# Optimization experiments

Hardware: AMD Instinct MI355X
Metric: run time of the kernel (lower is better)

Reference implementation:

```python
import jax, jax.numpy as jnp
import numpy as np

B, T, IN, H, OUT = 16384, 60, 1, 50, 1


def setup_inputs() -> dict:
    key = jax.random.key(0)
    ks = jax.random.split(key, 7)
    s = 1.0 / np.sqrt(H)
    return {
        "input_seq": jax.random.normal(ks[0], (B, T, IN), dtype=jnp.float32),
        "w_ih": jax.random.uniform(ks[1], (4 * H, IN), jnp.float32, -s, s),
        "w_hh": jax.random.uniform(ks[2], (4 * H, H), jnp.float32, -s, s),
        "b_ih": jax.random.uniform(ks[3], (4 * H,), jnp.float32, -s, s),
        "b_hh": jax.random.uniform(ks[4], (4 * H,), jnp.float32, -s, s),
        "w_lin": jax.random.uniform(ks[5], (OUT, H * T), jnp.float32, -s, s),
        "b_lin": jax.random.uniform(ks[6], (OUT,), jnp.float32, -s, s),
    }


def reference(input_seq, w_ih, w_hh, b_ih, b_hh, w_lin, b_lin):
    # Precompute input projections for all timesteps: [T, B, 4H]
    x_proj = jnp.einsum('bti,gi->tbg', input_seq, w_ih) + b_ih + b_hh

    def step(carry, xp):
        h, c = carry
        gates = xp + h @ w_hh.T  # [B, 4H]
        i, f, g, o = jnp.split(gates, 4, axis=-1)  # PyTorch gate order
        i, f, o = jax.nn.sigmoid(i), jax.nn.sigmoid(f), jax.nn.sigmoid(o)
        g = jnp.tanh(g)
        c = f * c + i * g
        h = o * jnp.tanh(c)
        return (h, c), h

    h0 = jnp.zeros((input_seq.shape[0], H), dtype=input_seq.dtype)
    (_, _), hs = jax.lax.scan(step, (h0, h0), x_proj)  # hs: [T, B, H]
    lstm_out = jnp.transpose(hs, (1, 0, 2)).reshape(-1, H * T)  # [B, T*H]
    return lstm_out @ w_lin.T + b_lin
```

## Files before the change

### kernel.cpp

```cpp
#include <hip/hip_runtime.h>


namespace {
constexpr int TS = 60;

typedef _Float16 half8 __attribute__((ext_vector_type(8)));
typedef _Float16 half2v __attribute__((ext_vector_type(2)));
typedef float f32x4 __attribute__((ext_vector_type(4)));

__device__ __forceinline__ float fexp2(float x) { return __builtin_amdgcn_exp2f(x); }
__device__ __forceinline__ float frcp(float x) { return __builtin_amdgcn_rcpf(x); }
__device__ __forceinline__ f32x4 mfma16(half8 a, half8 b, f32x4 c) {
  return __builtin_amdgcn_mfma_f32_16x16x32_f16(a, b, c, 0, 0, 0);
}
}

__global__ __launch_bounds__(256, 2) void lstm_t13(
    const float* __restrict__ x,
    const float* __restrict__ w_ih,
    const float* __restrict__ w_hh,
    const float* __restrict__ b_ih,
    const float* __restrict__ b_hh,
    const float* __restrict__ w_lin,
    const float* __restrict__ b_lin,
    float* __restrict__ out)
{
  __shared__ __align__(16) _Float16 Hs[2][2][16 * 64];
  __shared__ float WL[TS * 64];
  __shared__ float XL[TS * 32];
  __shared__ float OB[4][2][16];

  const int tid = threadIdx.x;
  const int lane = tid & 63;
  const int wv = tid >> 6;
  const int g = lane >> 4;
  const int cl = lane & 15;
  const int s8 = cl & 7;
  const long bbase = (long)blockIdx.x * 32;

  for (int i = tid; i < TS * 32; i += 256) {
    const int b = i / TS, t = i - b * TS;
    XL[t * 32 + b] = x[bbase * TS + i];
  }
  for (int i = tid; i < TS * 64; i += 256) {
    const int t = i >> 6, u = i & 63;
    WL[i] = (u < 50) ? w_lin[t * 50 + u] : 0.0f;
  }
  for (int i = tid; i < 2048; i += 256) ((unsigned*)Hs)[i] = 0u;

  half8 A[4][2];
  {
    const int gate = cl & 3, du = cl >> 2;
    const int ntile = (wv < 3) ? 4 : 1;
#pragma unroll
    for (int tau = 0; tau < 4; ++tau) {
      const int T = (wv < 3) ? (4 * wv + tau) : 12;
      const int uA = 4 * T + du;
      const int orig = gate * 50 + uA;
      const bool valid = (tau < ntile) && (uA < 50);
#pragma unroll
      for (int kc = 0; kc < 2; ++kc) {
        half8 fr;
#pragma unroll
        for (int e = 0; e < 8; ++e) {
          const int k = kc * 32 + 8 * g + e;
          float v = 0.0f;
          if (valid) {
            if (k < 50) v = w_hh[orig * 50 + k];
            else if (k == 62) v = b_ih[orig] + b_hh[orig];
            else if (k == 63) v = w_ih[orig];
          }
          fr[e] = (_Float16)v;
        }
        A[tau][kc] = fr;
      }
    }
  }
  __syncthreads();

  if (wv == 3 && g == 3) {
#pragma unroll
    for (int grp = 0; grp < 2; ++grp) {
      const half2v sp = {(_Float16)1.0f, (_Float16)XL[grp * 16 + cl]};
      *(half2v*)&Hs[grp][0][cl * 64 + ((7 ^ s8) << 3) + 6] = sp;
    }
  }
  __syncthreads();

  const int rh0 = cl * 64 + ((g ^ s8) << 3);
  const int rh1 = cl * 64 + (((4 | g) ^ s8) << 3);

  float c[2][4] = {{0.f, 0.f, 0.f, 0.f}, {0.f, 0.f, 0.f, 0.f}};
  float oacc[2] = {0.f, 0.f};

  constexpr float L1 = 1.4426950408889634f;
  constexpr float L2 = 2.8853900817779268f;

#define DO_TILES(NT, TBASE)                                                   \
  {                                                                           \
    f32x4 acc[2][NT];                                                         \
    _Pragma("unroll") for (int grp = 0; grp < 2; ++grp) {                     \
      _Pragma("unroll") for (int tau = 0; tau < NT; ++tau) {                  \
        f32x4 a = {0.f, 0.f, 0.f, 0.f};                                       \
        a = mfma16(A[tau][0], grp ? B0b : B0a, a);                            \
        a = mfma16(A[tau][1], grp ? B1b : B1a, a);                            \
        acc[grp][tau] = a;                                                    \
      }                                                                       \
    }                                                                         \
    _Pragma("unroll") for (int tau = 0; tau < NT; ++tau) {                    \
      const int u = 4 * (TBASE + tau) + g;                                    \
      const float wlv = WL[t * 64 + u];                                       \
      const int widx = cl * 64 + (((u >> 3) ^ s8) << 3) + (u & 7);            \
      _Pragma("unroll") for (int grp = 0; grp < 2; ++grp) {                   \
        const float E1 = fexp2(-L1 * acc[grp][tau][0]);                       \
        const float E2 = fexp2(-L1 * acc[grp][tau][1]);                       \
        const float E3 = fexp2(-L1 * acc[grp][tau][3]);                       \
        const float E4 = fexp2(L2 * acc[grp][tau][2]);                        \
        const float P1 = 1.0f + E1, P2 = 1.0f + E2;                           \
        const float P3 = 1.0f + E3, P4 = 1.0f + E4;                           \
        const float p12 = P1 * P2, p34 = P3 * P4;                             \
        const float r = frcp(p12 * p34);                                      \
        const float r12 = r * p34, r34 = r * p12;                             \
        const float si = r12 * P2, sf = r12 * P1, so = r34 * P4;              \
        const float tg = fmaf(-2.0f, r34 * P3, 1.0f);                         \
        const float cn = fmaf(sf, c[grp][tau], si * tg);                      \
        c[grp][tau] = cn;                                                     \
        const float Ec = fexp2(L2 * cn);                                      \
        const float tc = fmaf(-2.0f, frcp(1.0f + Ec), 1.0f);                  \
        const float hn = so * tc;                                             \
        oacc[grp] = fmaf(hn, wlv, oacc[grp]);                                 \
        (grp ? HN1 : HN0)[widx] = (_Float16)hn;                               \
      }                                                                       \
    }                                                                         \
  }

#pragma unroll 1
  for (int t = 0; t < TS; ++t) {
    const int p = t & 1;
    const _Float16* HR0 = &Hs[0][p][0];
    const _Float16* HR1 = &Hs[1][p][0];
    _Float16* HN0 = &Hs[0][p ^ 1][0];
    _Float16* HN1 = &Hs[1][p ^ 1][0];
    const half8 B0a = *(const half8*)&HR0[rh0];
    const half8 B1a = *(const half8*)&HR0[rh1];
    const half8 B0b = *(const half8*)&HR1[rh0];
    const half8 B1b = *(const half8*)&HR1[rh1];

    if (wv < 3) {
      const int tb = 4 * wv;
      DO_TILES(4, tb);
    } else {
      DO_TILES(1, 12);
      if (g == 3) {
        const int tn = (t + 1 < TS) ? (t + 1) : (TS - 1);
        const half2v spa = {(_Float16)1.0f, (_Float16)XL[tn * 32 + cl]};
        const half2v spb = {(_Float16)1.0f, (_Float16)XL[tn * 32 + 16 + cl]};
        *(half2v*)&HN0[cl * 64 + ((7 ^ s8) << 3) + 6] = spa;
        *(half2v*)&HN1[cl * 64 + ((7 ^ s8) << 3) + 6] = spb;
      }
    }
    __syncthreads();
  }
#undef DO_TILES

  oacc[0] += __shfl_xor(oacc[0], 32);
  oacc[0] += __shfl_xor(oacc[0], 16);
  oacc[1] += __shfl_xor(oacc[1], 32);
  oacc[1] += __shfl_xor(oacc[1], 16);
  if (lane < 16) {
    OB[wv][0][cl] = oacc[0];
    OB[wv][1][cl] = oacc[1];
  }
  __syncthreads();
  if (tid < 32) {
    const int grp = tid >> 4, b = tid & 15;
    float s = b_lin[0];
#pragma unroll
    for (int q = 0; q < 4; ++q) s += OB[q][grp][b];
    out[bbase + grp * 16 + b] = s;
  }
}

extern "C" void kernel_launch(void* const* d_in, const int* in_sizes, int n_in,
                              void* d_out, int out_size, void* d_ws, size_t ws_size,
                              hipStream_t stream) {
  const float* x     = (const float*)d_in[0];
  const float* w_ih  = (const float*)d_in[1];
  const float* w_hh  = (const float*)d_in[2];
  const float* b_ih  = (const float*)d_in[3];
  const float* b_hh  = (const float*)d_in[4];
  const float* w_lin = (const float*)d_in[5];
  const float* b_lin = (const float*)d_in[6];
  float* out = (float*)d_out;

  dim3 grid(16384 / 32);
  dim3 block(256);
  lstm_t13<<<grid, block, 0, stream>>>(x, w_ih, w_hh, b_ih, b_hh, w_lin,
                                       b_lin, out);
}
```

Measured before the change: 91.35 us.

## Balance gate tiles across waves and halve batch per block

Result: slower. 97.90 us (+7.2%).

```diff
diff --git a/kernel.cpp b/kernel.cpp
--- a/kernel.cpp
+++ b/kernel.cpp
@@ -15,7 +15,7 @@
 }
 }
 
-__global__ __launch_bounds__(256, 2) void lstm_t13(
+__global__ __launch_bounds__(256, 4) void lstm_bal(
     const float* __restrict__ x,
     const float* __restrict__ w_ih,
     const float* __restrict__ w_hh,
@@ -25,10 +25,10 @@
     const float* __restrict__ b_lin,
     float* __restrict__ out)
 {
-  __shared__ __align__(16) _Float16 Hs[2][2][16 * 64];
+  __shared__ __align__(16) _Float16 Hs[2][16 * 64];
   __shared__ float WL[TS * 64];
-  __shared__ float XL[TS * 32];
-  __shared__ float OB[4][2][16];
+  __shared__ float XL[TS * 16];
+  __shared__ float OB[4][16];
 
   const int tid = threadIdx.x;
   const int lane = tid & 63;
@@ -36,25 +36,29 @@
   const int g = lane >> 4;
   const int cl = lane & 15;
   const int s8 = cl & 7;
-  const long bbase = (long)blockIdx.x * 32;
+  const int bid = blockIdx.x;
+  const long bbase = (long)bid * 16;
 
-  for (int i = tid; i < TS * 32; i += 256) {
+  const int hv = (bid + (bid >> 8)) & 3;
+  const int ntile = 3 + (wv == hv);
+  const int tbase = 3 * wv + (wv > hv ? 1 : 0);
+
+  for (int i = tid; i < TS * 16; i += 256) {
     const int b = i / TS, t = i - b * TS;
-    XL[t * 32 + b] = x[bbase * TS + i];
+    XL[t * 16 + b] = x[bbase * TS + i];
   }
   for (int i = tid; i < TS * 64; i += 256) {
     const int t = i >> 6, u = i & 63;
     WL[i] = (u < 50) ? w_lin[t * 50 + u] : 0.0f;
   }
-  for (int i = tid; i < 2048; i += 256) ((unsigned*)Hs)[i] = 0u;
+  for (int i = tid; i < 1024; i += 256) ((unsigned*)Hs)[i] = 0u;
 
   half8 A[4][2];
   {
     const int gate = cl & 3, du = cl >> 2;
-    const int ntile = (wv < 3) ? 4 : 1;
 #pragma unroll
     for (int tau = 0; tau < 4; ++tau) {
-      const int T = (wv < 3) ? (4 * wv + tau) : 12;
+      const int T = tbase + tau;
       const int uA = 4 * T + du;
       const int orig = gate * 50 + uA;
       const bool valid = (tau < ntile) && (uA < 50);
@@ -79,105 +83,85 @@
   __syncthreads();
 
   if (wv == 3 && g == 3) {
-#pragma unroll
-    for (int grp = 0; grp < 2; ++grp) {
-      const half2v sp = {(_Float16)1.0f, (_Float16)XL[grp * 16 + cl]};
-      *(half2v*)&Hs[grp][0][cl * 64 + ((7 ^ s8) << 3) + 6] = sp;
-    }
+    const half2v sp = {(_Float16)1.0f, (_Float16)XL[cl]};
+    *(half2v*)&Hs[0][cl * 64 + ((7 ^ s8) << 3) + 6] = sp;
   }
   __syncthreads();
 
   const int rh0 = cl * 64 + ((g ^ s8) << 3);
   const int rh1 = cl * 64 + (((4 | g) ^ s8) << 3);
 
-  float c[2][4] = {{0.f, 0.f, 0.f, 0.f}, {0.f, 0.f, 0.f, 0.f}};
-  float oacc[2] = {0.f, 0.f};
+  float c[4] = {0.f, 0.f, 0.f, 0.f};
+  float oacc = 0.0f;
 
   constexpr float L1 = 1.4426950408889634f;
   constexpr float L2 = 2.8853900817779268f;
 
-#define DO_TILES(NT, TBASE)                                                   \
+#define DO_TILES(NT)                                                          \
   {                                                                           \
-    f32x4 acc[2][NT];                                                         \
-    _Pragma("unroll") for (int grp = 0; grp < 2; ++grp) {                     \
-      _Pragma("unroll") for (int tau = 0; tau < NT; ++tau) {                  \
-        f32x4 a = {0.f, 0.f, 0.f, 0.f};                                       \
-        a = mfma16(A[tau][0], grp ? B0b : B0a, a);                            \
-        a = mfma16(A[tau][1], grp ? B1b : B1a, a);                            \
-        acc[grp][tau] = a;                                                    \
-      }                                                                       \
+    f32x4 acc[NT];                                                            \
+    _Pragma("unroll") for (int tau = 0; tau < NT; ++tau) {                    \
+      f32x4 a = {0.f, 0.f, 0.f, 0.f};                                         \
+      a = mfma16(A[tau][0], B0, a);                                           \
+      a = mfma16(A[tau][1], B1, a);                                           \
+      acc[tau] = a;                                                           \
     }                                                                         \
     _Pragma("unroll") for (int tau = 0; tau < NT; ++tau) {                    \
-      const int u = 4 * (TBASE + tau) + g;                                    \
+      const int u = 4 * (tbase + tau) + g;                                    \
       const float wlv = WL[t * 64 + u];                                       \
       const int widx = cl * 64 + (((u >> 3) ^ s8) << 3) + (u & 7);            \
-      _Pragma("unroll") for (int grp = 0; grp < 2; ++grp) {                   \
-        const float E1 = fexp2(-L1 * acc[grp][tau][0]);                       \
-        const float E2 = fexp2(-L1 * acc[grp][tau][1]);                       \
-        const float E3 = fexp2(-L1 * acc[grp][tau][3]);                       \
-        const float E4 = fexp2(L2 * acc[grp][tau][2]);                        \
-        const float P1 = 1.0f + E1, P2 = 1.0f + E2;                           \
-        const float P3 = 1.0f + E3, P4 = 1.0f + E4;                           \
-        const float p12 = P1 * P2, p34 = P3 * P4;                             \
-        const float r = frcp(p12 * p34);                                      \
-        const float r12 = r * p34, r34 = r * p12;                             \
-        const float si = r12 * P2, sf = r12 * P1, so = r34 * P4;              \
-        const float tg = fmaf(-2.0f, r34 * P3, 1.0f);                         \
-        const float cn = fmaf(sf, c[grp][tau], si * tg);                      \
-        c[grp][tau] = cn;                                                     \
-        const float Ec = fexp2(L2 * cn);                                      \
-        const float tc = fmaf(-2.0f, frcp(1.0f + Ec), 1.0f);                  \
-        const float hn = so * tc;                                             \
-        oacc[grp] = fmaf(hn, wlv, oacc[grp]);                                 \
-        (grp ? HN1 : HN0)[widx] = (_Float16)hn;                               \
-      }                                                                       \
+      const float E1 = fexp2(-L1 * acc[tau][0]);                              \
+      const float E2 = fexp2(-L1 * acc[tau][1]);                              \
+      const float E3 = fexp2(-L1 * acc[tau][3]);                              \
+      const float E4 = fexp2(L2 * acc[tau][2]);                               \
+      const float P1 = 1.0f + E1, P2 = 1.0f + E2;                             \
+      const float P3 = 1.0f + E3, P4 = 1.0f + E4;                             \
+      const float p12 = P1 * P2, p34 = P3 * P4;                               \
+      const float r = frcp(p12 * p34);                                        \
+      const float r12 = r * p34, r34 = r * p12;                               \
+      const float si = r12 * P2, sf = r12 * P1, so = r34 * P4;                \
+      const float tg = fmaf(-2.0f, r34 * P3, 1.0f);                           \
+      const float cn = fmaf(sf, c[tau], si * tg);                             \
+      c[tau] = cn;                                                            \
+      const float Ec = fexp2(L2 * cn);                                        \
+      const float tc = fmaf(-2.0f, frcp(1.0f + Ec), 1.0f);                    \
+      const float hn = so * tc;                                               \
+      oacc = fmaf(hn, wlv, oacc);                                             \
+      HW[widx] = (_Float16)hn;                                                \
     }                                                                         \
   }
 
 #pragma unroll 1
   for (int t = 0; t < TS; ++t) {
     const int p = t & 1;
-    const _Float16* HR0 = &Hs[0][p][0];
-    const _Float16* HR1 = &Hs[1][p][0];
-    _Float16* HN0 = &Hs[0][p ^ 1][0];
-    _Float16* HN1 = &Hs[1][p ^ 1][0];
-    const half8 B0a = *(const half8*)&HR0[rh0];
-    const half8 B1a = *(const half8*)&HR0[rh1];
-    const half8 B0b = *(const half8*)&HR1[rh0];
-    const half8 B1b = *(const half8*)&HR1[rh1];
+    const _Float16* HR = &Hs[p][0];
+    _Float16* HW = &Hs[p ^ 1][0];
+    const half8 B0 = *(const half8*)&HR[rh0];
+    const half8 B1 = *(const half8*)&HR[rh1];
 
-    if (wv < 3) {
-      const int tb = 4 * wv;
-      DO_TILES(4, tb);
+    if (wv == hv) {
+      DO_TILES(4);
     } else {
-      DO_TILES(1, 12);
-      if (g == 3) {
-        const int tn = (t + 1 < TS) ? (t + 1) : (TS - 1);
-        const half2v spa = {(_Float16)1.0f, (_Float16)XL[tn * 32 + cl]};
-        const half2v spb = {(_Float16)1.0f, (_Float16)XL[tn * 32 + 16 + cl]};
-        *(half2v*)&HN0[cl * 64 + ((7 ^ s8) << 3) + 6] = spa;
-        *(half2v*)&HN1[cl * 64 + ((7 ^ s8) << 3) + 6] = spb;
-      }
+      DO_TILES(3);
+    }
+    if (wv == 3 && g == 3) {
+      const int tn = (t + 1 < TS) ? (t + 1) : (TS - 1);
+      const half2v sp = {(_Float16)1.0f, (_Float16)XL[tn * 16 + cl]};
+      *(half2v*)&HW[cl * 64 + ((7 ^ s8) << 3) + 6] = sp;
     }
     __syncthreads();
   }
 #undef DO_TILES
 
-  oacc[0] += __shfl_xor(oacc[0], 32);
-  oacc[0] += __shfl_xor(oacc[0], 16);
-  oacc[1] += __shfl_xor(oacc[1], 32);
-  oacc[1] += __shfl_xor(oacc[1], 16);
-  if (lane < 16) {
-    OB[wv][0][cl] = oacc[0];
-    OB[wv][1][cl] = oacc[1];
-  }
+  oacc += __shfl_xor(oacc, 32);
+  oacc += __shfl_xor(oacc, 16);
+  if (lane < 16) OB[wv][cl] = oacc;
   __syncthreads();
-  if (tid < 32) {
-    const int grp = tid >> 4, b = tid & 15;
+  if (tid < 16) {
     float s = b_lin[0];
 #pragma unroll
-    for (int q = 0; q < 4; ++q) s += OB[q][grp][b];
-    out[bbase + grp * 16 + b] = s;
+    for (int q = 0; q < 4; ++q) s += OB[q][tid];
+    out[bbase + tid] = s;
   }
 }
 
@@ -193,8 +177,8 @@
   const float* b_lin = (const float*)d_in[6];
   float* out = (float*)d_out;
 
-  dim3 grid(16384 / 32);
+  dim3 grid(16384 / 16);
   dim3 block(256);
-  lstm_t13<<<grid, block, 0, stream>>>(x, w_ih, w_hh, b_ih, b_hh, w_lin,
+  lstm_bal<<<grid, block, 0, stream>>>(x, w_ih, w_hh, b_ih, b_hh, w_lin,
                                        b_lin, out);
 }
```

## Balance gate tiles across waves, polynomial exp2, shared reciprocal across groups

Applied to the files above, without the earlier changes.

Result: slower. 132.9 us (+45.5%).

```diff
diff --git a/kernel.cpp b/kernel.cpp
--- a/kernel.cpp
+++ b/kernel.cpp
@@ -8,14 +8,26 @@
 typedef _Float16 half2v __attribute__((ext_vector_type(2)));
 typedef float f32x4 __attribute__((ext_vector_type(4)));
 
-__device__ __forceinline__ float fexp2(float x) { return __builtin_amdgcn_exp2f(x); }
 __device__ __forceinline__ float frcp(float x) { return __builtin_amdgcn_rcpf(x); }
+
+__device__ __forceinline__ float pexp2(float x) {
+  const float t = __builtin_rintf(x);
+  const float f = x - t;
+  float p = 9.6181291e-3f;
+  p = fmaf(p, f, 5.5504109e-2f);
+  p = fmaf(p, f, 2.4022651e-1f);
+  p = fmaf(p, f, 6.9314718e-1f);
+  p = fmaf(p, f, 1.0f);
+  const int n = (int)t;
+  const float s = __builtin_bit_cast(float, (n + 127) << 23);
+  return p * s;
+}
 __device__ __forceinline__ f32x4 mfma16(half8 a, half8 b, f32x4 c) {
   return __builtin_amdgcn_mfma_f32_16x16x32_f16(a, b, c, 0, 0, 0);
 }
 }
 
-__global__ __launch_bounds__(256, 2) void lstm_t13(
+__global__ __launch_bounds__(256, 2) void lstm_poly(
     const float* __restrict__ x,
     const float* __restrict__ w_ih,
     const float* __restrict__ w_hh,
@@ -36,7 +48,12 @@
   const int g = lane >> 4;
   const int cl = lane & 15;
   const int s8 = cl & 7;
-  const long bbase = (long)blockIdx.x * 32;
+  const int bid = blockIdx.x;
+  const long bbase = (long)bid * 32;
+
+  const int hv = bid & 3;
+  const int ntile = 3 + (wv == hv);
+  const int tbase = 3 * wv + (wv > hv ? 1 : 0);
 
   for (int i = tid; i < TS * 32; i += 256) {
     const int b = i / TS, t = i - b * TS;
@@ -51,10 +68,9 @@
   half8 A[4][2];
   {
     const int gate = cl & 3, du = cl >> 2;
-    const int ntile = (wv < 3) ? 4 : 1;
 #pragma unroll
     for (int tau = 0; tau < 4; ++tau) {
-      const int T = (wv < 3) ? (4 * wv + tau) : 12;
+      const int T = tbase + tau;
       const int uA = 4 * T + du;
       const int orig = gate * 50 + uA;
       const bool valid = (tau < ntile) && (uA < 50);
@@ -90,49 +106,12 @@
   const int rh0 = cl * 64 + ((g ^ s8) << 3);
   const int rh1 = cl * 64 + (((4 | g) ^ s8) << 3);
 
-  float c[2][4] = {{0.f, 0.f, 0.f, 0.f}, {0.f, 0.f, 0.f, 0.f}};
-  float oacc[2] = {0.f, 0.f};
+  float c0[4] = {0.f, 0.f, 0.f, 0.f};
+  float c1[4] = {0.f, 0.f, 0.f, 0.f};
+  float oacc0 = 0.f, oacc1 = 0.f;
 
   constexpr float L1 = 1.4426950408889634f;
   constexpr float L2 = 2.8853900817779268f;
-
-#define DO_TILES(NT, TBASE)                                                   \
-  {                                                                           \
-    f32x4 acc[2][NT];                                                         \
-    _Pragma("unroll") for (int grp = 0; grp < 2; ++grp) {                     \
-      _Pragma("unroll") for (int tau = 0; tau < NT; ++tau) {                  \
-        f32x4 a = {0.f, 0.f, 0.f, 0.f};                                       \
-        a = mfma16(A[tau][0], grp ? B0b : B0a, a);                            \
-        a = mfma16(A[tau][1], grp ? B1b : B1a, a);                            \
-        acc[grp][tau] = a;                                                    \
-      }                                                                       \
-    }                                                                         \
-    _Pragma("unroll") for (int tau = 0; tau < NT; ++tau) {                    \
-      const int u = 4 * (TBASE + tau) + g;                                    \
-      const float wlv = WL[t * 64 + u];                                       \
-      const int widx = cl * 64 + (((u >> 3) ^ s8) << 3) + (u & 7);            \
-      _Pragma("unroll") for (int grp = 0; grp < 2; ++grp) {                   \
-        const float E1 = fexp2(-L1 * acc[grp][tau][0]);                       \
-        const float E2 = fexp2(-L1 * acc[grp][tau][1]);                       \
-        const float E3 = fexp2(-L1 * acc[grp][tau][3]);                       \
-        const float E4 = fexp2(L2 * acc[grp][tau][2]);                        \
-        const float P1 = 1.0f + E1, P2 = 1.0f + E2;                           \
-        const float P3 = 1.0f + E3, P4 = 1.0f + E4;                           \
-        const float p12 = P1 * P2, p34 = P3 * P4;                             \
-        const float r = frcp(p12 * p34);                                      \
-        const float r12 = r * p34, r34 = r * p12;                             \
-        const float si = r12 * P2, sf = r12 * P1, so = r34 * P4;              \
-        const float tg = fmaf(-2.0f, r34 * P3, 1.0f);                         \
-        const float cn = fmaf(sf, c[grp][tau], si * tg);                      \
-        c[grp][tau] = cn;                                                     \
-        const float Ec = fexp2(L2 * cn);                                      \
-        const float tc = fmaf(-2.0f, frcp(1.0f + Ec), 1.0f);                  \
-        const float hn = so * tc;                                             \
-        oacc[grp] = fmaf(hn, wlv, oacc[grp]);                                 \
-        (grp ? HN1 : HN0)[widx] = (_Float16)hn;                               \
-      }                                                                       \
-    }                                                                         \
-  }
 
 #pragma unroll 1
   for (int t = 0; t < TS; ++t) {
@@ -146,30 +125,82 @@
     const half8 B0b = *(const half8*)&HR1[rh0];
     const half8 B1b = *(const half8*)&HR1[rh1];
 
-    if (wv < 3) {
-      const int tb = 4 * wv;
-      DO_TILES(4, tb);
-    } else {
-      DO_TILES(1, 12);
-      if (g == 3) {
-        const int tn = (t + 1 < TS) ? (t + 1) : (TS - 1);
-        const half2v spa = {(_Float16)1.0f, (_Float16)XL[tn * 32 + cl]};
-        const half2v spb = {(_Float16)1.0f, (_Float16)XL[tn * 32 + 16 + cl]};
-        *(half2v*)&HN0[cl * 64 + ((7 ^ s8) << 3) + 6] = spa;
-        *(half2v*)&HN1[cl * 64 + ((7 ^ s8) << 3) + 6] = spb;
+    f32x4 da[4], db[4];
+#pragma unroll
+    for (int tau = 0; tau < 4; ++tau) {
+      if (tau < ntile) {
+        f32x4 z = {0.f, 0.f, 0.f, 0.f};
+        da[tau] = mfma16(A[tau][1], B1a, mfma16(A[tau][0], B0a, z));
+        db[tau] = mfma16(A[tau][1], B1b, mfma16(A[tau][0], B0b, z));
       }
     }
+
+#pragma unroll
+    for (int tau = 0; tau < 4; ++tau) {
+      if (tau < ntile) {
+        const int u = 4 * (tbase + tau) + g;
+        const float wlv = WL[t * 64 + u];
+        const int widx = cl * 64 + (((u >> 3) ^ s8) << 3) + (u & 7);
+        const float E1a = pexp2(-L1 * da[tau][0]);
+        const float E2a = pexp2(-L1 * da[tau][1]);
+        const float E3a = pexp2(-L1 * da[tau][3]);
+        const float E4a = pexp2(L2 * da[tau][2]);
+        const float P1a = 1.0f + E1a, P2a = 1.0f + E2a;
+        const float P3a = 1.0f + E3a, P4a = 1.0f + E4a;
+        const float p12a = P1a * P2a, p34a = P3a * P4a;
+        const float pra = p12a * p34a;
+        const float E1b = pexp2(-L1 * db[tau][0]);
+        const float E2b = pexp2(-L1 * db[tau][1]);
+        const float E3b = pexp2(-L1 * db[tau][3]);
+        const float E4b = pexp2(L2 * db[tau][2]);
+        const float P1b = 1.0f + E1b, P2b = 1.0f + E2b;
+        const float P3b = 1.0f + E3b, P4b = 1.0f + E4b;
+        const float p12b = P1b * P2b, p34b = P3b * P4b;
+        const float prb = p12b * p34b;
+        const float R = frcp(pra * prb);
+        const float ra = R * prb, rb = R * pra;
+        const float r12a = ra * p34a, r34a = ra * p12a;
+        const float sia = r12a * P2a, sfa = r12a * P1a, soa = r34a * P4a;
+        const float tga = fmaf(-2.0f, r34a * P3a, 1.0f);
+        const float cna = fmaf(sfa, c0[tau], sia * tga);
+        c0[tau] = cna;
+        const float r12b = rb * p34b, r34b = rb * p12b;
+        const float sib = r12b * P2b, sfb = r12b * P1b, sob = r34b * P4b;
+        const float tgb = fmaf(-2.0f, r34b * P3b, 1.0f);
+        const float cnb = fmaf(sfb, c1[tau], sib * tgb);
+        c1[tau] = cnb;
+        const float aca = fminf(fmaxf(L2 * cna, -14.5f), 14.5f);
+        const float acb = fminf(fmaxf(L2 * cnb, -14.5f), 14.5f);
+        const float Pca = 1.0f + pexp2(aca);
+        const float Pcb = 1.0f + pexp2(acb);
+        const float Rc = frcp(Pca * Pcb);
+        const float tca = fmaf(-2.0f, Rc * Pcb, 1.0f);
+        const float tcb = fmaf(-2.0f, Rc * Pca, 1.0f);
+        const float hna = soa * tca;
+        const float hnb = sob * tcb;
+        oacc0 = fmaf(hna, wlv, oacc0);
+        oacc1 = fmaf(hnb, wlv, oacc1);
+        HN0[widx] = (_Float16)hna;
+        HN1[widx] = (_Float16)hnb;
+      }
+    }
+    if (wv == 3 && g == 3) {
+      const int tn = (t + 1 < TS) ? (t + 1) : (TS - 1);
+      const half2v spa = {(_Float16)1.0f, (_Float16)XL[tn * 32 + cl]};
+      const half2v spb = {(_Float16)1.0f, (_Float16)XL[tn * 32 + 16 + cl]};
+      *(half2v*)&HN0[cl * 64 + ((7 ^ s8) << 3) + 6] = spa;
+      *(half2v*)&HN1[cl * 64 + ((7 ^ s8) << 3) + 6] = spb;
+    }
     __syncthreads();
   }
-#undef DO_TILES
-
-  oacc[0] += __shfl_xor(oacc[0], 32);
-  oacc[0] += __shfl_xor(oacc[0], 16);
-  oacc[1] += __shfl_xor(oacc[1], 32);
-  oacc[1] += __shfl_xor(oacc[1], 16);
+
+  oacc0 += __shfl_xor(oacc0, 32);
+  oacc0 += __shfl_xor(oacc0, 16);
+  oacc1 += __shfl_xor(oacc1, 32);
+  oacc1 += __shfl_xor(oacc1, 16);
   if (lane < 16) {
-    OB[wv][0][cl] = oacc[0];
-    OB[wv][1][cl] = oacc[1];
+    OB[wv][0][cl] = oacc0;
+    OB[wv][1][cl] = oacc1;
   }
   __syncthreads();
   if (tid < 32) {
@@ -195,6 +226,6 @@
 
   dim3 grid(16384 / 32);
   dim3 block(256);
-  lstm_t13<<<grid, block, 0, stream>>>(x, w_ih, w_hh, b_ih, b_hh, w_lin,
-                                       b_lin, out);
-}
+  lstm_poly<<<grid, block, 0, stream>>>(x, w_ih, w_hh, b_ih, b_hh, w_lin,
+                                        b_lin, out);
+}
```
